# Kernel optimization log

Hardware: AMD Instinct MI355X
Metric: run time of the kernel (lower is better)

Reference implementation:

```python
import jax, jax.numpy as jnp
import numpy as np

N_NODES = 50000
N_SCHEMES = 5
K = 16
HIDDEN = 128
N_CLASSES = 8


def setup_inputs() -> dict:
    key = jax.random.key(0)
    ks = jax.random.split(key, 8)
    sc_nei = jax.random.randint(ks[0], (N_SCHEMES, N_NODES, K), 0, N_NODES)
    feats = jax.random.normal(ks[1], (N_NODES, HIDDEN), dtype=jnp.float32)
    W1 = jax.random.normal(ks[2], (HIDDEN, HIDDEN), dtype=jnp.float32) * (1.0 / np.sqrt(HIDDEN))
    b1 = jnp.zeros((HIDDEN,), dtype=jnp.float32)
    W2 = jax.random.normal(ks[3], (HIDDEN, N_CLASSES), dtype=jnp.float32) * (1.0 / np.sqrt(HIDDEN))
    b2 = jnp.zeros((N_CLASSES,), dtype=jnp.float32)
    alpha = jax.random.normal(ks[4], (N_NODES, 1), dtype=jnp.float32)
    attention = jax.random.normal(ks[5], (N_NODES, N_SCHEMES, 1), dtype=jnp.float32)
    return {"sc_nei": sc_nei, "feats": feats, "W1": W1, "b1": b1,
            "W2": W2, "b2": b2, "alpha": alpha, "attention": attention}


def _mlp(x, W1, b1, W2, b2):
    # MLP2 with num_layers=2, dropout in eval mode (identity)
    h = jax.nn.relu(x @ W1 + b1)
    return h @ W2 + b2


def reference(sc_nei, feats, W1, b1, W2, b2, alpha, attention):
    # Per-scheme: gather -> MLP -> exp(log_softmax)=softmax -> mean over neighbors
    emb = feats[sc_nei]                      # [5, N, K, H]
    probs = jax.nn.softmax(_mlp(emb, W1, b1, W2, b2), axis=-1)  # [5, N, K, C]
    sc_cls = probs.mean(axis=2)              # [5, N, C]
    x = jnp.moveaxis(sc_cls, 0, -1)          # [N, C, 5]
    att = jax.nn.softmax(attention, axis=1)  # [N, 5, 1]
    scheme_pred = jnp.squeeze(x @ att, -1)   # [N, C]
    self_pred = jax.nn.softmax(_mlp(feats[:N_NODES], W1, b1, W2, b2), axis=-1)  # [N, C]
    gate = jax.nn.sigmoid(alpha)             # sigmoid(-a) = 1 - sigmoid(a)
    return gate * self_pred + (1.0 - gate) * scheme_pred
```

## Files before the change

### kernel.cpp

```cpp
#include <hip/hip_runtime.h>
#include <math.h>

#define HIDDEN   128
#define NCLS     8
#define NSCHEMES 5
#define KNEI     16

#define MT   64
#define KC   32
#define ASTR 36
#define WSTR 136

__global__ __launch_bounds__(256) void mlp_probs(
    const float* __restrict__ feats, const float* __restrict__ W1,
    const float* __restrict__ b1, const float* __restrict__ W2,
    const float* __restrict__ b2, float* __restrict__ probs, int N)
{
    __shared__ float Ach[MT * ASTR];
    __shared__ float Wc[KC * WSTR];
    __shared__ float W2lds[HIDDEN * NCLS];
    __shared__ float b1v[HIDDEN];
    __shared__ float b2v[NCLS];

    const int tid = threadIdx.x;
    const int nodeBase = blockIdx.x * MT;
    const int n0 = tid & 15;
    const int j0 = tid >> 4;

    {
        float4 v = ((const float4*)W2)[tid];
        *(float4*)&W2lds[4 * tid] = v;
    }
    if (tid < HIDDEN) b1v[tid] = b1[tid];
    if (tid < NCLS)   b2v[tid] = b2[tid];

    float acc[4][8];
    #pragma unroll
    for (int r = 0; r < 4; ++r)
        #pragma unroll
        for (int j = 0; j < 8; ++j) acc[r][j] = 0.f;

    for (int kc = 0; kc < HIDDEN; kc += KC) {
        #pragma unroll
        for (int idx = tid; idx < MT * KC / 4; idx += 256) {
            int r = idx >> 3, c4 = idx & 7;
            int n = nodeBase + r; if (n >= N) n = N - 1;
            float4 v = ((const float4*)(feats + (size_t)n * HIDDEN + kc))[c4];
            *(float4*)&Ach[r * ASTR + 4 * c4] = v;
        }
        #pragma unroll
        for (int idx = tid; idx < KC * HIDDEN / 4; idx += 256) {
            int i = idx >> 5, c4 = idx & 31;
            float4 v = ((const float4*)(W1 + (size_t)(kc + i) * HIDDEN))[c4];
            *(float4*)&Wc[i * WSTR + 4 * c4] = v;
        }
        __syncthreads();

        #pragma unroll
        for (int k = 0; k < KC; k += 4) {
            float4 a[4];
            #pragma unroll
            for (int r = 0; r < 4; ++r)
                a[r] = *(const float4*)&Ach[(n0 + 16 * r) * ASTR + k];
            float4 w[4][2];
            #pragma unroll
            for (int kk = 0; kk < 4; ++kk) {
                w[kk][0] = *(const float4*)&Wc[(k + kk) * WSTR + 8 * j0];
                w[kk][1] = *(const float4*)&Wc[(k + kk) * WSTR + 8 * j0 + 4];
            }
            #pragma unroll
            for (int r = 0; r < 4; ++r) {
                float av[4] = {a[r].x, a[r].y, a[r].z, a[r].w};
                #pragma unroll
                for (int kk = 0; kk < 4; ++kk) {
                    acc[r][0] = fmaf(av[kk], w[kk][0].x, acc[r][0]);
                    acc[r][1] = fmaf(av[kk], w[kk][0].y, acc[r][1]);
                    acc[r][2] = fmaf(av[kk], w[kk][0].z, acc[r][2]);
                    acc[r][3] = fmaf(av[kk], w[kk][0].w, acc[r][3]);
                    acc[r][4] = fmaf(av[kk], w[kk][1].x, acc[r][4]);
                    acc[r][5] = fmaf(av[kk], w[kk][1].y, acc[r][5]);
                    acc[r][6] = fmaf(av[kk], w[kk][1].z, acc[r][6]);
                    acc[r][7] = fmaf(av[kk], w[kk][1].w, acc[r][7]);
                }
            }
        }
        __syncthreads();
    }

    {
        float4 bA = *(const float4*)&b1v[8 * j0];
        float4 bB = *(const float4*)&b1v[8 * j0 + 4];
        float bb[8] = {bA.x, bA.y, bA.z, bA.w, bB.x, bB.y, bB.z, bB.w};
        #pragma unroll
        for (int r = 0; r < 4; ++r)
            #pragma unroll
            for (int j = 0; j < 8; ++j)
                acc[r][j] = fmaxf(acc[r][j] + bb[j], 0.f);
    }

    float o[4][NCLS];
    #pragma unroll
    for (int r = 0; r < 4; ++r)
        #pragma unroll
        for (int c = 0; c < NCLS; ++c) o[r][c] = 0.f;

    #pragma unroll
    for (int jj = 0; jj < 8; ++jj) {
        float4 w0 = *(const float4*)&W2lds[(8 * j0 + jj) * NCLS];
        float4 w1 = *(const float4*)&W2lds[(8 * j0 + jj) * NCLS + 4];
        #pragma unroll
        for (int r = 0; r < 4; ++r) {
            float h = acc[r][jj];
            o[r][0] = fmaf(h, w0.x, o[r][0]);
            o[r][1] = fmaf(h, w0.y, o[r][1]);
            o[r][2] = fmaf(h, w0.z, o[r][2]);
            o[r][3] = fmaf(h, w0.w, o[r][3]);
            o[r][4] = fmaf(h, w1.x, o[r][4]);
            o[r][5] = fmaf(h, w1.y, o[r][5]);
            o[r][6] = fmaf(h, w1.z, o[r][6]);
            o[r][7] = fmaf(h, w1.w, o[r][7]);
        }
    }

    #pragma unroll
    for (int r = 0; r < 4; ++r)
        #pragma unroll
        for (int c = 0; c < NCLS; ++c) {
            float v = o[r][c];
            v += __shfl_xor(v, 16, 64);
            v += __shfl_xor(v, 32, 64);
            o[r][c] = v;
        }

    float* Red = Wc;
    const int wv = tid >> 6;
    if ((tid & 48) == 0) {
        #pragma unroll
        for (int r = 0; r < 4; ++r) {
            int node = n0 + 16 * r;
            float* dst = &Red[(wv * MT + node) * 12];
            *(float4*)dst       = make_float4(o[r][0], o[r][1], o[r][2], o[r][3]);
            *(float4*)(dst + 4) = make_float4(o[r][4], o[r][5], o[r][6], o[r][7]);
        }
    }
    __syncthreads();

    if (tid < MT) {
        int n = nodeBase + tid;
        if (n < N) {
            float oo[NCLS];
            #pragma unroll
            for (int c = 0; c < NCLS; ++c) oo[c] = b2v[c];
            #pragma unroll
            for (int w = 0; w < 4; ++w) {
                float4 p0 = *(const float4*)&Red[(w * MT + tid) * 12];
                float4 p1 = *(const float4*)&Red[(w * MT + tid) * 12 + 4];
                oo[0] += p0.x; oo[1] += p0.y; oo[2] += p0.z; oo[3] += p0.w;
                oo[4] += p1.x; oo[5] += p1.y; oo[6] += p1.z; oo[7] += p1.w;
            }
            float m = oo[0];
            #pragma unroll
            for (int c = 1; c < NCLS; ++c) m = fmaxf(m, oo[c]);
            float s = 0.f;
            #pragma unroll
            for (int c = 0; c < NCLS; ++c) { oo[c] = __expf(oo[c] - m); s += oo[c]; }
            float inv = 1.f / s;
            float4* op = (float4*)(probs + (size_t)n * NCLS);
            op[0] = make_float4(oo[0] * inv, oo[1] * inv, oo[2] * inv, oo[3] * inv);
            op[1] = make_float4(oo[4] * inv, oo[5] * inv, oo[6] * inv, oo[7] * inv);
        }
    }
}

__global__ __launch_bounds__(256) void combine(
    const int* __restrict__ nei, const float* __restrict__ probs,
    const float* __restrict__ attention, const float* __restrict__ alpha,
    float* __restrict__ out, int N)
{
    int t = blockIdx.x * 256 + threadIdx.x;
    int n = t >> 3;
    int c = t & 7;
    if (n >= N) return;

    float aw[NSCHEMES];
    float m = -1e30f;
    #pragma unroll
    for (int s = 0; s < NSCHEMES; ++s) {
        aw[s] = attention[(size_t)n * NSCHEMES + s];
        m = fmaxf(m, aw[s]);
    }
    float ssum = 0.f;
    #pragma unroll
    for (int s = 0; s < NSCHEMES; ++s) { aw[s] = __expf(aw[s] - m); ssum += aw[s]; }
    float invs = 1.f / ssum;

    float acc = 0.f;
    #pragma unroll
    for (int s = 0; s < NSCHEMES; ++s) {
        const int* ip = nei + ((size_t)s * N + n) * KNEI;
        int4 q0 = ((const int4*)ip)[0];
        int4 q1 = ((const int4*)ip)[1];
        int4 q2 = ((const int4*)ip)[2];
        int4 q3 = ((const int4*)ip)[3];
        float p[KNEI];
        p[ 0] = probs[(size_t)q0.x * NCLS + c];
        p[ 1] = probs[(size_t)q0.y * NCLS + c];
        p[ 2] = probs[(size_t)q0.z * NCLS + c];
        p[ 3] = probs[(size_t)q0.w * NCLS + c];
        p[ 4] = probs[(size_t)q1.x * NCLS + c];
        p[ 5] = probs[(size_t)q1.y * NCLS + c];
        p[ 6] = probs[(size_t)q1.z * NCLS + c];
        p[ 7] = probs[(size_t)q1.w * NCLS + c];
        p[ 8] = probs[(size_t)q2.x * NCLS + c];
        p[ 9] = probs[(size_t)q2.y * NCLS + c];
        p[10] = probs[(size_t)q2.z * NCLS + c];
        p[11] = probs[(size_t)q2.w * NCLS + c];
        p[12] = probs[(size_t)q3.x * NCLS + c];
        p[13] = probs[(size_t)q3.y * NCLS + c];
        p[14] = probs[(size_t)q3.z * NCLS + c];
        p[15] = probs[(size_t)q3.w * NCLS + c];
        float sum = ((p[0] + p[1]) + (p[2] + p[3])) + ((p[4] + p[5]) + (p[6] + p[7]))
                  + ((p[8] + p[9]) + (p[10] + p[11])) + ((p[12] + p[13]) + (p[14] + p[15]));
        acc = fmaf(aw[s] * invs * (1.f / (float)KNEI), sum, acc);
    }

    float g = 1.f / (1.f + __expf(-alpha[n]));
    float self = probs[(size_t)n * NCLS + c];
    out[t] = g * self + (1.f - g) * acc;
}

extern "C" void kernel_launch(void* const* d_in, const int* in_sizes, int n_in,
                              void* d_out, int out_size, void* d_ws, size_t ws_size,
                              hipStream_t stream) {
    const int*   sc_nei    = (const int*)d_in[0];
    const float* feats     = (const float*)d_in[1];
    const float* W1        = (const float*)d_in[2];
    const float* b1        = (const float*)d_in[3];
    const float* W2        = (const float*)d_in[4];
    const float* b2        = (const float*)d_in[5];
    const float* alpha     = (const float*)d_in[6];
    const float* attention = (const float*)d_in[7];
    float* out = (float*)d_out;

    int N = in_sizes[1] / HIDDEN;

    float* probs = (float*)d_ws;

    mlp_probs<<<(N + MT - 1) / MT, 256, 0, stream>>>(feats, W1, b1, W2, b2, probs, N);
    combine<<<((N * NCLS) + 255) / 256, 256, 0, stream>>>(sc_nei, probs, attention, alpha, out, N);
}
```

Measured before the change: 141.1 us.

## Halve MLP node tile and vectorize neighbor gather with lane-split reduction

The MLP kernel's node tile drops from 64 to 32 rows, with launch bounds asking for 4 blocks per CU, so more blocks run and register pressure falls. The second MLP layer is restructured to process one row at a time. The combine kernel now has each of 8 lanes per node gather whole 8-class probability rows as two float4 loads for 10 of the 80 neighbours, then sums across lanes with shuffles. This replaces 16 scalar loads per scheme per class lane, so fewer, wider gather transactions are issued. The cost is extra shuffle reductions and a select chain, and W1 is re-staged per block twice as often.

```diff
diff --git a/kernel.cpp b/kernel.cpp
--- a/kernel.cpp
+++ b/kernel.cpp
@@ -6,12 +6,12 @@
 #define NSCHEMES 5
 #define KNEI     16
 
-#define MT   64
+#define MT   32
 #define KC   32
 #define ASTR 36
 #define WSTR 136
 
-__global__ __launch_bounds__(256) void mlp_probs(
+__global__ __launch_bounds__(256, 4) void mlp_probs(
     const float* __restrict__ feats, const float* __restrict__ W1,
     const float* __restrict__ b1, const float* __restrict__ W2,
     const float* __restrict__ b2, float* __restrict__ probs, int N)
@@ -34,16 +34,15 @@
     if (tid < HIDDEN) b1v[tid] = b1[tid];
     if (tid < NCLS)   b2v[tid] = b2[tid];
 
-    float acc[4][8];
-    #pragma unroll
-    for (int r = 0; r < 4; ++r)
+    float acc[2][8];
+    #pragma unroll
+    for (int r = 0; r < 2; ++r)
         #pragma unroll
         for (int j = 0; j < 8; ++j) acc[r][j] = 0.f;
 
     for (int kc = 0; kc < HIDDEN; kc += KC) {
-        #pragma unroll
-        for (int idx = tid; idx < MT * KC / 4; idx += 256) {
-            int r = idx >> 3, c4 = idx & 7;
+        {
+            int r = tid >> 3, c4 = tid & 7;
             int n = nodeBase + r; if (n >= N) n = N - 1;
             float4 v = ((const float4*)(feats + (size_t)n * HIDDEN + kc))[c4];
             *(float4*)&Ach[r * ASTR + 4 * c4] = v;
@@ -58,9 +57,9 @@
 
         #pragma unroll
         for (int k = 0; k < KC; k += 4) {
-            float4 a[4];
-            #pragma unroll
-            for (int r = 0; r < 4; ++r)
+            float4 a[2];
+            #pragma unroll
+            for (int r = 0; r < 2; ++r)
                 a[r] = *(const float4*)&Ach[(n0 + 16 * r) * ASTR + k];
             float4 w[4][2];
             #pragma unroll
@@ -69,7 +68,7 @@
                 w[kk][1] = *(const float4*)&Wc[(k + kk) * WSTR + 8 * j0 + 4];
             }
             #pragma unroll
-            for (int r = 0; r < 4; ++r) {
+            for (int r = 0; r < 2; ++r) {
                 float av[4] = {a[r].x, a[r].y, a[r].z, a[r].w};
                 #pragma unroll
                 for (int kk = 0; kk < 4; ++kk) {
@@ -92,55 +91,45 @@
         float4 bB = *(const float4*)&b1v[8 * j0 + 4];
         float bb[8] = {bA.x, bA.y, bA.z, bA.w, bB.x, bB.y, bB.z, bB.w};
         #pragma unroll
-        for (int r = 0; r < 4; ++r)
+        for (int r = 0; r < 2; ++r)
             #pragma unroll
             for (int j = 0; j < 8; ++j)
                 acc[r][j] = fmaxf(acc[r][j] + bb[j], 0.f);
     }
 
-    float o[4][NCLS];
-    #pragma unroll
-    for (int r = 0; r < 4; ++r)
-        #pragma unroll
-        for (int c = 0; c < NCLS; ++c) o[r][c] = 0.f;
-
-    #pragma unroll
-    for (int jj = 0; jj < 8; ++jj) {
-        float4 w0 = *(const float4*)&W2lds[(8 * j0 + jj) * NCLS];
-        float4 w1 = *(const float4*)&W2lds[(8 * j0 + jj) * NCLS + 4];
-        #pragma unroll
-        for (int r = 0; r < 4; ++r) {
+    float* Red = Wc;
+    const int wv = tid >> 6;
+    #pragma unroll
+    for (int r = 0; r < 2; ++r) {
+        float o[NCLS];
+        #pragma unroll
+        for (int c = 0; c < NCLS; ++c) o[c] = 0.f;
+        #pragma unroll
+        for (int jj = 0; jj < 8; ++jj) {
+            float4 w0 = *(const float4*)&W2lds[(8 * j0 + jj) * NCLS];
+            float4 w1 = *(const float4*)&W2lds[(8 * j0 + jj) * NCLS + 4];
             float h = acc[r][jj];
-            o[r][0] = fmaf(h, w0.x, o[r][0]);
-            o[r][1] = fmaf(h, w0.y, o[r][1]);
-            o[r][2] = fmaf(h, w0.z, o[r][2]);
-            o[r][3] = fmaf(h, w0.w, o[r][3]);
-            o[r][4] = fmaf(h, w1.x, o[r][4]);
-            o[r][5] = fmaf(h, w1.y, o[r][5]);
-            o[r][6] = fmaf(h, w1.z, o[r][6]);
-            o[r][7] = fmaf(h, w1.w, o[r][7]);
-        }
-    }
-
-    #pragma unroll
-    for (int r = 0; r < 4; ++r)
+            o[0] = fmaf(h, w0.x, o[0]);
+            o[1] = fmaf(h, w0.y, o[1]);
+            o[2] = fmaf(h, w0.z, o[2]);
+            o[3] = fmaf(h, w0.w, o[3]);
+            o[4] = fmaf(h, w1.x, o[4]);
+            o[5] = fmaf(h, w1.y, o[5]);
+            o[6] = fmaf(h, w1.z, o[6]);
+            o[7] = fmaf(h, w1.w, o[7]);
+        }
         #pragma unroll
         for (int c = 0; c < NCLS; ++c) {
-            float v = o[r][c];
+            float v = o[c];
             v += __shfl_xor(v, 16, 64);
             v += __shfl_xor(v, 32, 64);
-            o[r][c] = v;
-        }
-
-    float* Red = Wc;
-    const int wv = tid >> 6;
-    if ((tid & 48) == 0) {
-        #pragma unroll
-        for (int r = 0; r < 4; ++r) {
+            o[c] = v;
+        }
+        if ((tid & 48) == 0) {
             int node = n0 + 16 * r;
             float* dst = &Red[(wv * MT + node) * 12];
-            *(float4*)dst       = make_float4(o[r][0], o[r][1], o[r][2], o[r][3]);
-            *(float4*)(dst + 4) = make_float4(o[r][4], o[r][5], o[r][6], o[r][7]);
+            *(float4*)dst       = make_float4(o[0], o[1], o[2], o[3]);
+            *(float4*)(dst + 4) = make_float4(o[4], o[5], o[6], o[7]);
         }
     }
     __syncthreads();
@@ -179,7 +168,7 @@
 {
     int t = blockIdx.x * 256 + threadIdx.x;
     int n = t >> 3;
-    int c = t & 7;
+    int L = t & 7;
     if (n >= N) return;
 
     float aw[NSCHEMES];
@@ -192,41 +181,49 @@
     float ssum = 0.f;
     #pragma unroll
     for (int s = 0; s < NSCHEMES; ++s) { aw[s] = __expf(aw[s] - m); ssum += aw[s]; }
-    float invs = 1.f / ssum;
-
-    float acc = 0.f;
-    #pragma unroll
-    for (int s = 0; s < NSCHEMES; ++s) {
-        const int* ip = nei + ((size_t)s * N + n) * KNEI;
-        int4 q0 = ((const int4*)ip)[0];
-        int4 q1 = ((const int4*)ip)[1];
-        int4 q2 = ((const int4*)ip)[2];
-        int4 q3 = ((const int4*)ip)[3];
-        float p[KNEI];
-        p[ 0] = probs[(size_t)q0.x * NCLS + c];
-        p[ 1] = probs[(size_t)q0.y * NCLS + c];
-        p[ 2] = probs[(size_t)q0.z * NCLS + c];
-        p[ 3] = probs[(size_t)q0.w * NCLS + c];
-        p[ 4] = probs[(size_t)q1.x * NCLS + c];
-        p[ 5] = probs[(size_t)q1.y * NCLS + c];
-        p[ 6] = probs[(size_t)q1.z * NCLS + c];
-        p[ 7] = probs[(size_t)q1.w * NCLS + c];
-        p[ 8] = probs[(size_t)q2.x * NCLS + c];
-        p[ 9] = probs[(size_t)q2.y * NCLS + c];
-        p[10] = probs[(size_t)q2.z * NCLS + c];
-        p[11] = probs[(size_t)q2.w * NCLS + c];
-        p[12] = probs[(size_t)q3.x * NCLS + c];
-        p[13] = probs[(size_t)q3.y * NCLS + c];
-        p[14] = probs[(size_t)q3.z * NCLS + c];
-        p[15] = probs[(size_t)q3.w * NCLS + c];
-        float sum = ((p[0] + p[1]) + (p[2] + p[3])) + ((p[4] + p[5]) + (p[6] + p[7]))
-                  + ((p[8] + p[9]) + (p[10] + p[11])) + ((p[12] + p[13]) + (p[14] + p[15]));
-        acc = fmaf(aw[s] * invs * (1.f / (float)KNEI), sum, acc);
-    }
 
     float g = 1.f / (1.f + __expf(-alpha[n]));
-    float self = probs[(size_t)n * NCLS + c];
-    out[t] = g * self + (1.f - g) * acc;
+    float scale = (1.f - g) / (ssum * (float)KNEI);
+    float wn[NSCHEMES];
+    #pragma unroll
+    for (int s = 0; s < NSCHEMES; ++s) wn[s] = aw[s] * scale;
+
+    float acc[NCLS];
+    #pragma unroll
+    for (int c = 0; c < NCLS; ++c) acc[c] = 0.f;
+
+    #pragma unroll
+    for (int mm = 0; mm < 10; ++mm) {
+        int s = mm >> 1;
+        int k = ((mm & 1) << 3) + L;
+        int id = nei[((size_t)s * N + n) * KNEI + k];
+        const float4* pp = (const float4*)(probs + (size_t)id * NCLS);
+        float4 p0 = pp[0], p1 = pp[1];
+        float w = wn[s];
+        acc[0] = fmaf(w, p0.x, acc[0]);
+        acc[1] = fmaf(w, p0.y, acc[1]);
+        acc[2] = fmaf(w, p0.z, acc[2]);
+        acc[3] = fmaf(w, p0.w, acc[3]);
+        acc[4] = fmaf(w, p1.x, acc[4]);
+        acc[5] = fmaf(w, p1.y, acc[5]);
+        acc[6] = fmaf(w, p1.z, acc[6]);
+        acc[7] = fmaf(w, p1.w, acc[7]);
+    }
+
+    #pragma unroll
+    for (int c = 0; c < NCLS; ++c) {
+        float v = acc[c];
+        v += __shfl_xor(v, 1, 64);
+        v += __shfl_xor(v, 2, 64);
+        v += __shfl_xor(v, 4, 64);
+        acc[c] = v;
+    }
+
+    float self = probs[(size_t)n * NCLS + L];
+    float res = acc[0];
+    #pragma unroll
+    for (int c = 1; c < NCLS; ++c) res = (L == c) ? acc[c] : res;
+    out[t] = fmaf(g, self, res);
 }
 
 extern "C" void kernel_launch(void* const* d_in, const int* in_sizes, int n_in,
```

Result: no change. 140.3 us (-0.6%).
